# Kernel tuning notes

Measured on AMD Instinct MI355X. Metric: run time of the kernel, lower is better.

## Reference

```python
import jax, jax.numpy as jnp
import numpy as np
import math

SCALE = 64.0
MARGIN = 0.5
EPS = 1e-07
COS_M = math.cos(MARGIN)
SIN_M = math.sin(MARGIN)
THRESHOLD = math.cos(math.pi - MARGIN)
MM = math.sin(math.pi - MARGIN) * MARGIN

N, D, C = 512, 512, 100000


def setup_inputs() -> dict:
    key = jax.random.key(0)
    k1, k2, k3 = jax.random.split(key, 3)
    x = jax.random.normal(k1, (N, D), dtype=jnp.float32)
    weight = jax.random.normal(k2, (C, D), dtype=jnp.float32)
    t = jnp.zeros((1,), dtype=jnp.float32)
    target = jax.random.randint(k3, (N,), 0, C, dtype=jnp.int64)
    return {"x": x, "weight": weight, "t": t, "target": target}


def reference(x, weight, t, target):
    # normalized linear -> cosine similarities [N, C]
    xn = x / jnp.linalg.norm(x, axis=1, keepdims=True)
    wn = weight / jnp.linalg.norm(weight, axis=1, keepdims=True)
    cos_theta = jnp.clip(jnp.einsum('nd,cd->nc', xn, wn), -1.0 + EPS, 1.0 - EPS)

    rows = jnp.arange(cos_theta.shape[0])
    target_logit = cos_theta[rows, target][:, None]            # [N, 1]
    sin_theta = jnp.sqrt(1.0 - target_logit * target_logit)
    cos_theta_m = target_logit * COS_M - sin_theta * SIN_M      # cos(theta + m)

    mask = cos_theta > cos_theta_m                              # hard examples
    final_target_logit = jnp.where(target_logit > THRESHOLD,
                                   cos_theta_m,
                                   target_logit - MM)

    # EMA buffer update (no-grad in torch)
    t_new = jax.lax.stop_gradient(target_logit.mean() * 0.01 + 0.99 * t)  # [1]

    # hard-example re-weighting: cos * (t + cos) where mask
    cos_theta = jnp.where(mask, cos_theta * (t_new[0] + cos_theta), cos_theta)
    # scatter margin-adjusted target logit into target column
    cos_theta = cos_theta.at[rows, target].set(final_target_logit[:, 0])

    logits = cos_theta * SCALE
    # cross entropy (mean)
    logp = jax.nn.log_softmax(logits, axis=-1)
    loss = -jnp.mean(logp[rows, target])
    return loss
```

## Files before the change

### kernel.cpp

```cpp
#include <hip/hip_runtime.h>
#include <hip/hip_bf16.h>
#include <stdint.h>

#define N_ROWS 512
#define D_DIM  512
#define C_CLS  100000

#define SCALE_F    64.0f
#define EPS_F      1e-7f
#define COS_M_F    0.8775825618903728f
#define SIN_M_F    0.4794255386042030f
#define THRESH_F  -0.8775825618903728f
#define MM_F       0.2397127693021015f
#define FIXMAX_F   65.0f

#define NC  64
#define NG2 1564

#define XN8_OFF    0
#define TL_OFF     (XN8_OFF + 512*512)
#define CTM_OFF    (TL_OFF + 2048)
#define FTL_OFF    (CTM_OFF + 2048)
#define TNEW_OFF   (FTL_OFF + 2048)
#define XNORM_OFF  (TNEW_OFF + 256)
#define PSUM_OFF   (XNORM_OFF + 2048)
#define LOSSI_OFF  (PSUM_OFF + NG2*512*4)

typedef __attribute__((ext_vector_type(4))) float f32x4;

#define GLOAD_LDS16(gp, lp) \
    __builtin_amdgcn_global_load_lds((const __attribute__((address_space(1))) void*)(gp), \
                                     (__attribute__((address_space(3))) void*)(lp), 16, 0, 0)

#if defined(__has_builtin)
#if __has_builtin(__builtin_amdgcn_cvt_pk_fp8_f32)
#define HAVE_CVT_FP8 1
#endif
#endif

__device__ inline unsigned char f2e4m3(float f) {
    union { float f; unsigned u; } a; a.f = f;
    unsigned s = (a.u >> 24) & 0x80u;
    float af = fabsf(f);
    if (af < 0.015625f) {
        int q = (int)(af * 512.0f + 0.5f);
        return (unsigned char)(s | (unsigned)q);
    }
    unsigned x = a.u & 0x7FFFFFFFu;
    unsigned r = x + 0x000FFFFFu + ((x >> 20) & 1u);
    int ec = (int)(r >> 23) - 127 + 7;
    unsigned m = (r >> 20) & 7u;
    if (ec > 15 || (ec == 15 && m == 7u)) return (unsigned char)(s | 0x7Eu);
    return (unsigned char)(s | ((unsigned)ec << 3) | m);
}

__device__ inline unsigned pack4_fp8(float f0, float f1, float f2, float f3) {
#ifdef HAVE_CVT_FP8
    int q = __builtin_amdgcn_cvt_pk_fp8_f32(f0, f1, 0, false);
    q     = __builtin_amdgcn_cvt_pk_fp8_f32(f2, f3, q, true);
    return (unsigned)q;
#else
    union { unsigned char b[4]; unsigned u; } u;
    u.b[0]=f2e4m3(f0); u.b[1]=f2e4m3(f1); u.b[2]=f2e4m3(f2); u.b[3]=f2e4m3(f3);
    return u.u;
#endif
}

__device__ inline uint2 pack8_fp8(float f0, float f1, float f2, float f3,
                                  float f4, float f5, float f6, float f7) {
    uint2 r;
    r.x = pack4_fp8(f0, f1, f2, f3);
    r.y = pack4_fp8(f4, f5, f6, f7);
    return r;
}

__device__ inline float wave_sum64(float v) {
    #pragma unroll
    for (int m = 1; m < 64; m <<= 1) v += __shfl_xor(v, m);
    return v;
}

__global__ void k_xnorm_fp8(const float* __restrict__ x,
                            unsigned char* __restrict__ xn8,
                            float* __restrict__ xnorm) {
    int row = blockIdx.x;
    int lane = threadIdx.x;
    const float* xr = x + row * D_DIM + lane * 8;
    float4 v0 = *(const float4*)(xr);
    float4 v1 = *(const float4*)(xr + 4);
    float s = v0.x*v0.x + v0.y*v0.y + v0.z*v0.z + v0.w*v0.w
            + v1.x*v1.x + v1.y*v1.y + v1.z*v1.z + v1.w*v1.w;
    s = wave_sum64(s);
    float nrm = sqrtf(s);
    if (lane == 0) xnorm[row] = nrm;
    float inv = 1.0f / nrm;
    uint2 q = pack8_fp8(v0.x*inv, v0.y*inv, v0.z*inv, v0.w*inv,
                        v1.x*inv, v1.y*inv, v1.z*inv, v1.w*inv);
    *(uint2*)(xn8 + row * D_DIM + lane * 8) = q;
}

__global__ void k_tlogit(const float* __restrict__ x, const float* __restrict__ w,
                         const float* __restrict__ xnorm,
                         const int* __restrict__ target,
                         float* __restrict__ tl, float* __restrict__ ctm,
                         float* __restrict__ ftl) {
    int row = blockIdx.x;
    int lane = threadIdx.x;
    int tgt = target[row];
    const float* xr = x + row * D_DIM + lane * 8;
    const float* wr = w + (size_t)tgt * D_DIM + lane * 8;
    float4 a0 = *(const float4*)(xr),     a1 = *(const float4*)(xr + 4);
    float4 b0 = *(const float4*)(wr),     b1 = *(const float4*)(wr + 4);
    float s = a0.x*b0.x + a0.y*b0.y + a0.z*b0.z + a0.w*b0.w
            + a1.x*b1.x + a1.y*b1.y + a1.z*b1.z + a1.w*b1.w;
    float q = b0.x*b0.x + b0.y*b0.y + b0.z*b0.z + b0.w*b0.w
            + b1.x*b1.x + b1.y*b1.y + b1.z*b1.z + b1.w*b1.w;
    s = wave_sum64(s);
    q = wave_sum64(q);
    if (lane == 0) {
        float c = s / (xnorm[row] * sqrtf(q));
        c = fminf(fmaxf(c, -1.0f + EPS_F), 1.0f - EPS_F);
        float sn = sqrtf(fmaxf(1.0f - c * c, 0.0f));
        float cm = c * COS_M_F - sn * SIN_M_F;
        tl[row]  = c;
        ctm[row] = cm;
        ftl[row] = (c > THRESH_F) ? cm : (c - MM_F);
    }
}

__global__ void k_tnew(const float* __restrict__ tl, const float* __restrict__ t,
                       float* __restrict__ tnew) {
    __shared__ float s[512];
    int tid = threadIdx.x;
    s[tid] = tl[tid];
    __syncthreads();
    for (int off = 256; off > 0; off >>= 1) {
        if (tid < off) s[tid] += s[tid + off];
        __syncthreads();
    }
    if (tid == 0) tnew[0] = (s[0] / 512.0f) * 0.01f + 0.99f * t[0];
}

__global__ __launch_bounds__(512, 4) void k_fused(
        const unsigned char* __restrict__ xn8,
        const float* __restrict__ w,
        const int* __restrict__ target,
        const float* __restrict__ ctm,
        const float* __restrict__ ftl,
        const float* __restrict__ tnew,
        float* __restrict__ psum) {
    __shared__ unsigned char As[2][512 * 64];
    __shared__ unsigned char Bs[2][64 * 64];
    __shared__ float invS[64];
    __shared__ int   tgt_s[512];
    __shared__ float ctm_s[512];
    __shared__ float ftl_s[512];

    int bx = blockIdx.x;
    int cb = bx * NC;
    int tid = threadIdx.x;
    int lane = tid & 63, wid = tid >> 6;
    int fr = lane & 15, rgrp = lane >> 4;
    int wrow = wid * 64;

    tgt_s[tid] = target[tid];
    ctm_s[tid] = ctm[tid];
    ftl_s[tid] = ftl[tid];
    float tn = tnew[0];

    int brow  = tid >> 3;
    int bslot = tid & 7;
    int bclass = cb + brow;
    bool brvalid = (bclass < C_CLS);
    const float* bsrc = w + (size_t)(brvalid ? bclass : 0) * D_DIM + bslot * 8;

    float sumsq = 0.0f;
    int bwaddr = brow * 64 + ((bslot * 8) ^ ((brow & 3) << 4));

    #define STAGE_A(kk, buf)                                                  \
        do {                                                                  \
            _Pragma("unroll")                                                 \
            for (int c = 0; c < 4; ++c) {                                     \
                int lo = c * 8192 + wid * 1024;             \
                int o  = lo + lane * 16;                                      \
                int row = o >> 6, b = o & 63;                                 \
                GLOAD_LDS16(xn8 + (size_t)row * 512 + (kk) * 64               \
                                + (b ^ ((row & 3) << 4)),                     \
                            (char*)As[buf] + lo);                             \
            }                                                                 \
        } while (0)

    #define WRITE_B(va, vb, buf)                                              \
        do {                                                                  \
            sumsq += va.x*va.x + va.y*va.y + va.z*va.z + va.w*va.w            \
                   + vb.x*vb.x + vb.y*vb.y + vb.z*vb.z + vb.w*vb.w;           \
            uint2 pk_;                                                        \
            pk_.x = pack4_fp8(va.x, va.y, va.z, va.w);                        \
            pk_.y = pack4_fp8(vb.x, vb.y, vb.z, vb.w);                        \
            *(uint2*)(&Bs[buf][bwaddr]) = pk_;                                \
        } while (0)

    __builtin_amdgcn_sched_barrier(0);
    float4 v0a = *(const float4*)(bsrc);
    float4 v0b = *(const float4*)(bsrc + 4);
    STAGE_A(0, 0);
    __builtin_amdgcn_sched_barrier(0);
    float4 rv_next0 = *(const float4*)(bsrc + 1 * 64);
    float4 rv_next1 = *(const float4*)(bsrc + 1 * 64 + 4);
    float4 rv_far0  = *(const float4*)(bsrc + 2 * 64);
    float4 rv_far1  = *(const float4*)(bsrc + 2 * 64 + 4);
    WRITE_B(v0a, v0b, 0);
    asm volatile("s_waitcnt vmcnt(4) lgkmcnt(0)" ::: "memory");
    __builtin_amdgcn_sched_barrier(0);
    __builtin_amdgcn_s_barrier();
    __builtin_amdgcn_sched_barrier(0);

    f32x4 acc[4][4];
    #pragma unroll
    for (int m = 0; m < 4; m++)
        #pragma unroll
        for (int j = 0; j < 4; j++)
            acc[m][j] = (f32x4){0.f, 0.f, 0.f, 0.f};

    union LL { uint2 u; long long ll; };
    int akey = (fr & 3) << 4;

    #pragma unroll
    for (int kk = 0; kk < 8; ++kk) {
        int cur = kk & 1;
        if (kk < 7) {
            STAGE_A(kk + 1, cur ^ 1);
            __builtin_amdgcn_sched_barrier(0);
            WRITE_B(rv_next0, rv_next1, cur ^ 1);
            rv_next0 = rv_far0;
            rv_next1 = rv_far1;
            if (kk < 5) {
                rv_far0 = *(const float4*)(bsrc + (kk + 3) * 64);
                rv_far1 = *(const float4*)(bsrc + (kk + 3) * 64 + 4);
            }
        }
        #pragma unroll
        for (int sub = 0; sub < 2; ++sub) {
            uint2 af[4], bf[4];
            int soff = (sub * 32 + rgrp * 8) ^ akey;
            #pragma unroll
            for (int m = 0; m < 4; m++)
                af[m] = *(const uint2*)(&As[cur][(wrow + m * 16 + fr) * 64 + soff]);
            #pragma unroll
            for (int j = 0; j < 4; j++)
                bf[j] = *(const uint2*)(&Bs[cur][(j * 16 + fr) * 64 + soff]);
            __builtin_amdgcn_s_setprio(1);
            #pragma unroll
            for (int m = 0; m < 4; m++)
                #pragma unroll
                for (int j = 0; j < 4; j++) {
                    LL a, b;
                    a.u = af[m];
                    b.u = bf[j];
                    acc[m][j] = __builtin_amdgcn_mfma_f32_16x16x32_fp8_fp8(
                                    a.ll, b.ll, acc[m][j], 0, 0, 0);
                }
            __builtin_amdgcn_s_setprio(0);
        }
        if (kk < 7) {
            if (kk < 5)
                asm volatile("s_waitcnt vmcnt(2) lgkmcnt(0)" ::: "memory");
            else
                asm volatile("s_waitcnt vmcnt(0) lgkmcnt(0)" ::: "memory");
            __builtin_amdgcn_sched_barrier(0);
            __builtin_amdgcn_s_barrier();
            __builtin_amdgcn_sched_barrier(0);
        }
    }
    #undef STAGE_A
    #undef WRITE_B

    float s2 = sumsq;
    s2 += __shfl_xor(s2, 1);
    s2 += __shfl_xor(s2, 2);
    s2 += __shfl_xor(s2, 4);
    if (bslot == 0) invS[brow] = rsqrtf(s2);
    __syncthreads();

    float inv[4];
    bool cvalid[4];
    #pragma unroll
    for (int j = 0; j < 4; j++) {
        inv[j] = invS[j * 16 + fr];
        cvalid[j] = (cb + j * 16 + fr) < C_CLS;
    }
    #pragma unroll
    for (int m = 0; m < 4; m++) {
        #pragma unroll
        for (int reg = 0; reg < 4; reg++) {
            int rl = wrow + m * 16 + rgrp * 4 + reg;
            int tr = tgt_s[rl];
            float cm = ctm_s[rl];
            float ft = ftl_s[rl];
            float sm = 0.0f;
            #pragma unroll
            for (int j = 0; j < 4; j++) {
                int col = cb + j * 16 + fr;
                float c = acc[m][j][reg] * inv[j];
                c = fminf(fmaxf(c, -1.0f + EPS_F), 1.0f - EPS_F);
                float v = (c > cm) ? c * (tn + c) : c;
                v *= SCALE_F;
                v = (col == tr) ? ft * SCALE_F : v;
                v = cvalid[j] ? v : -3.0e38f;
                sm += __expf(v - FIXMAX_F);
            }
            #pragma unroll
            for (int msk = 1; msk < 16; msk <<= 1) sm += __shfl_xor(sm, msk);
            if (fr == 0) psum[(size_t)bx * 512 + rl] = sm;
        }
    }
}

__global__ void k_rowlse_fix(const float* __restrict__ psum,
                             const float* __restrict__ ftl,
                             float* __restrict__ lossi) {
    int row = blockIdx.x, tid = threadIdx.x;
    float S = 0.0f;
    for (int nb = tid; nb < NG2; nb += 256) S += psum[(size_t)nb * 512 + row];
    __shared__ float sS[256];
    sS[tid] = S;
    __syncthreads();
    for (int off = 128; off > 0; off >>= 1) {
        if (tid < off) sS[tid] += sS[tid + off];
        __syncthreads();
    }
    if (tid == 0) lossi[row] = logf(sS[0]) + FIXMAX_F - SCALE_F * ftl[row];
}

__global__ void k_final(const float* __restrict__ lossi, float* __restrict__ out) {
    __shared__ float s[512];
    int tid = threadIdx.x;
    s[tid] = lossi[tid];
    __syncthreads();
    for (int off = 256; off > 0; off >>= 1) {
        if (tid < off) s[tid] += s[tid + off];
        __syncthreads();
    }
    if (tid == 0) out[0] = s[0] / 512.0f;
}

extern "C" void kernel_launch(void* const* d_in, const int* in_sizes, int n_in,
                              void* d_out, int out_size, void* d_ws, size_t ws_size,
                              hipStream_t stream) {
    const float* x      = (const float*)d_in[0];
    const float* w      = (const float*)d_in[1];
    const float* t      = (const float*)d_in[2];
    const int*   target = (const int*)d_in[3];

    char* ws = (char*)d_ws;
    unsigned char* xn8  = (unsigned char*)(ws + XN8_OFF);
    float* tl    = (float*)(ws + TL_OFF);
    float* ctm   = (float*)(ws + CTM_OFF);
    float* ftl   = (float*)(ws + FTL_OFF);
    float* tnew  = (float*)(ws + TNEW_OFF);
    float* xnorm = (float*)(ws + XNORM_OFF);
    float* psum  = (float*)(ws + PSUM_OFF);
    float* lossi = (float*)(ws + LOSSI_OFF);
    float* out   = (float*)d_out;

    k_xnorm_fp8<<<dim3(N_ROWS), dim3(64), 0, stream>>>(x, xn8, xnorm);
    k_tlogit<<<dim3(N_ROWS), dim3(64), 0, stream>>>(x, w, xnorm, target, tl, ctm, ftl);
    k_tnew<<<dim3(1), dim3(512), 0, stream>>>(tl, t, tnew);
    k_fused<<<dim3(NG2), dim3(512), 0, stream>>>(xn8, w, target, ctm, ftl, tnew, psum);
    k_rowlse_fix<<<dim3(N_ROWS), dim3(256), 0, stream>>>(psum, ftl, lossi);
    k_final<<<dim3(1), dim3(512), 0, stream>>>(lossi, out);
}
```

Measured before the change: 122.8 us.

## Merge prep kernels, fold EMA reduction into GEMM, pad B tile

Merges the x-normalisation and target-logit kernels into one prep kernel and drops the separate t_new reduction kernel. Each GEMM block now recomputes the mean of the target logits with wave reductions, which removes two launches and their serialisation gaps. The per-row target/ctm/ftl values are read from global memory in the epilogue instead of being staged in shared memory. The B tile switches from an XOR swizzle to a 72-byte padded row stride. The trade-off is redundant per-block reduction work and uncached-looking global loads in the epilogue.

```diff
diff --git a/kernel.cpp b/kernel.cpp
--- a/kernel.cpp
+++ b/kernel.cpp
@@ -21,9 +21,7 @@
 #define TL_OFF     (XN8_OFF + 512*512)
 #define CTM_OFF    (TL_OFF + 2048)
 #define FTL_OFF    (CTM_OFF + 2048)
-#define TNEW_OFF   (FTL_OFF + 2048)
-#define XNORM_OFF  (TNEW_OFF + 256)
-#define PSUM_OFF   (XNORM_OFF + 2048)
+#define PSUM_OFF   (FTL_OFF + 2048)
 #define LOSSI_OFF  (PSUM_OFF + NG2*512*4)
 
 typedef __attribute__((ext_vector_type(4))) float f32x4;
@@ -66,59 +64,43 @@
 #endif
 }
 
-__device__ inline uint2 pack8_fp8(float f0, float f1, float f2, float f3,
-                                  float f4, float f5, float f6, float f7) {
-    uint2 r;
-    r.x = pack4_fp8(f0, f1, f2, f3);
-    r.y = pack4_fp8(f4, f5, f6, f7);
-    return r;
-}
-
 __device__ inline float wave_sum64(float v) {
     #pragma unroll
     for (int m = 1; m < 64; m <<= 1) v += __shfl_xor(v, m);
     return v;
 }
 
-__global__ void k_xnorm_fp8(const float* __restrict__ x,
-                            unsigned char* __restrict__ xn8,
-                            float* __restrict__ xnorm) {
+__global__ void k_prep(const float* __restrict__ x, const float* __restrict__ w,
+                       const int* __restrict__ target,
+                       unsigned char* __restrict__ xn8,
+                       float* __restrict__ tl, float* __restrict__ ctm,
+                       float* __restrict__ ftl) {
     int row = blockIdx.x;
     int lane = threadIdx.x;
     const float* xr = x + row * D_DIM + lane * 8;
     float4 v0 = *(const float4*)(xr);
     float4 v1 = *(const float4*)(xr + 4);
-    float s = v0.x*v0.x + v0.y*v0.y + v0.z*v0.z + v0.w*v0.w
-            + v1.x*v1.x + v1.y*v1.y + v1.z*v1.z + v1.w*v1.w;
-    s = wave_sum64(s);
-    float nrm = sqrtf(s);
-    if (lane == 0) xnorm[row] = nrm;
+    float sx = v0.x*v0.x + v0.y*v0.y + v0.z*v0.z + v0.w*v0.w
+             + v1.x*v1.x + v1.y*v1.y + v1.z*v1.z + v1.w*v1.w;
+    sx = wave_sum64(sx);
+    float nrm = sqrtf(sx);
     float inv = 1.0f / nrm;
-    uint2 q = pack8_fp8(v0.x*inv, v0.y*inv, v0.z*inv, v0.w*inv,
-                        v1.x*inv, v1.y*inv, v1.z*inv, v1.w*inv);
-    *(uint2*)(xn8 + row * D_DIM + lane * 8) = q;
-}
-
-__global__ void k_tlogit(const float* __restrict__ x, const float* __restrict__ w,
-                         const float* __restrict__ xnorm,
-                         const int* __restrict__ target,
-                         float* __restrict__ tl, float* __restrict__ ctm,
-                         float* __restrict__ ftl) {
-    int row = blockIdx.x;
-    int lane = threadIdx.x;
+    uint2 q8;
+    q8.x = pack4_fp8(v0.x*inv, v0.y*inv, v0.z*inv, v0.w*inv);
+    q8.y = pack4_fp8(v1.x*inv, v1.y*inv, v1.z*inv, v1.w*inv);
+    *(uint2*)(xn8 + row * D_DIM + lane * 8) = q8;
+
     int tgt = target[row];
-    const float* xr = x + row * D_DIM + lane * 8;
     const float* wr = w + (size_t)tgt * D_DIM + lane * 8;
-    float4 a0 = *(const float4*)(xr),     a1 = *(const float4*)(xr + 4);
-    float4 b0 = *(const float4*)(wr),     b1 = *(const float4*)(wr + 4);
-    float s = a0.x*b0.x + a0.y*b0.y + a0.z*b0.z + a0.w*b0.w
-            + a1.x*b1.x + a1.y*b1.y + a1.z*b1.z + a1.w*b1.w;
+    float4 b0 = *(const float4*)(wr), b1 = *(const float4*)(wr + 4);
+    float s = v0.x*b0.x + v0.y*b0.y + v0.z*b0.z + v0.w*b0.w
+            + v1.x*b1.x + v1.y*b1.y + v1.z*b1.z + v1.w*b1.w;
     float q = b0.x*b0.x + b0.y*b0.y + b0.z*b0.z + b0.w*b0.w
             + b1.x*b1.x + b1.y*b1.y + b1.z*b1.z + b1.w*b1.w;
     s = wave_sum64(s);
     q = wave_sum64(q);
     if (lane == 0) {
-        float c = s / (xnorm[row] * sqrtf(q));
+        float c = s / (nrm * sqrtf(q));
         c = fminf(fmaxf(c, -1.0f + EPS_F), 1.0f - EPS_F);
         float sn = sqrtf(fmaxf(1.0f - c * c, 0.0f));
         float cm = c * COS_M_F - sn * SIN_M_F;
@@ -128,33 +110,18 @@
     }
 }
 
-__global__ void k_tnew(const float* __restrict__ tl, const float* __restrict__ t,
-                       float* __restrict__ tnew) {
-    __shared__ float s[512];
-    int tid = threadIdx.x;
-    s[tid] = tl[tid];
-    __syncthreads();
-    for (int off = 256; off > 0; off >>= 1) {
-        if (tid < off) s[tid] += s[tid + off];
-        __syncthreads();
-    }
-    if (tid == 0) tnew[0] = (s[0] / 512.0f) * 0.01f + 0.99f * t[0];
-}
-
 __global__ __launch_bounds__(512, 4) void k_fused(
         const unsigned char* __restrict__ xn8,
         const float* __restrict__ w,
         const int* __restrict__ target,
         const float* __restrict__ ctm,
         const float* __restrict__ ftl,
-        const float* __restrict__ tnew,
+        const float* __restrict__ tl,
+        const float* __restrict__ t,
         float* __restrict__ psum) {
     __shared__ unsigned char As[2][512 * 64];
-    __shared__ unsigned char Bs[2][64 * 64];
+    __shared__ unsigned char Bs[2][64 * 72];
     __shared__ float invS[64];
-    __shared__ int   tgt_s[512];
-    __shared__ float ctm_s[512];
-    __shared__ float ftl_s[512];
 
     int bx = blockIdx.x;
     int cb = bx * NC;
@@ -163,10 +130,19 @@
     int fr = lane & 15, rgrp = lane >> 4;
     int wrow = wid * 64;
 
-    tgt_s[tid] = target[tid];
-    ctm_s[tid] = ctm[tid];
-    ftl_s[tid] = ftl[tid];
-    float tn = tnew[0];
+    {
+        float v = tl[tid];
+        v = wave_sum64(v);
+        if (lane == 0) invS[wid] = v;
+    }
+    __syncthreads();
+    float tn;
+    {
+        float s8 = invS[0] + invS[1] + invS[2] + invS[3]
+                 + invS[4] + invS[5] + invS[6] + invS[7];
+        tn = (s8 / 512.0f) * 0.01f + 0.99f * t[0];
+    }
+    __syncthreads();
 
     int brow  = tid >> 3;
     int bslot = tid & 7;
@@ -175,7 +151,7 @@
     const float* bsrc = w + (size_t)(brvalid ? bclass : 0) * D_DIM + bslot * 8;
 
     float sumsq = 0.0f;
-    int bwaddr = brow * 64 + ((bslot * 8) ^ ((brow & 3) << 4));
+    int bwaddr = brow * 72 + bslot * 8;
 
     #define STAGE_A(kk, buf)                                                  \
         do {                                                                  \
@@ -243,12 +219,13 @@
         for (int sub = 0; sub < 2; ++sub) {
             uint2 af[4], bf[4];
             int soff = (sub * 32 + rgrp * 8) ^ akey;
+            int bcol = sub * 32 + rgrp * 8;
             #pragma unroll
             for (int m = 0; m < 4; m++)
                 af[m] = *(const uint2*)(&As[cur][(wrow + m * 16 + fr) * 64 + soff]);
             #pragma unroll
             for (int j = 0; j < 4; j++)
-                bf[j] = *(const uint2*)(&Bs[cur][(j * 16 + fr) * 64 + soff]);
+                bf[j] = *(const uint2*)(&Bs[cur][(j * 16 + fr) * 72 + bcol]);
             __builtin_amdgcn_s_setprio(1);
             #pragma unroll
             for (int m = 0; m < 4; m++)
@@ -294,9 +271,9 @@
         #pragma unroll
         for (int reg = 0; reg < 4; reg++) {
             int rl = wrow + m * 16 + rgrp * 4 + reg;
-            int tr = tgt_s[rl];
-            float cm = ctm_s[rl];
-            float ft = ftl_s[rl];
+            int tr = target[rl];
+            float cm = ctm[rl];
+            float ft = ftl[rl];
             float sm = 0.0f;
             #pragma unroll
             for (int j = 0; j < 4; j++) {
@@ -357,16 +334,12 @@
     float* tl    = (float*)(ws + TL_OFF);
     float* ctm   = (float*)(ws + CTM_OFF);
     float* ftl   = (float*)(ws + FTL_OFF);
-    float* tnew  = (float*)(ws + TNEW_OFF);
-    float* xnorm = (float*)(ws + XNORM_OFF);
     float* psum  = (float*)(ws + PSUM_OFF);
     float* lossi = (float*)(ws + LOSSI_OFF);
     float* out   = (float*)d_out;
 
-    k_xnorm_fp8<<<dim3(N_ROWS), dim3(64), 0, stream>>>(x, xn8, xnorm);
-    k_tlogit<<<dim3(N_ROWS), dim3(64), 0, stream>>>(x, w, xnorm, target, tl, ctm, ftl);
-    k_tnew<<<dim3(1), dim3(512), 0, stream>>>(tl, t, tnew);
-    k_fused<<<dim3(NG2), dim3(512), 0, stream>>>(xn8, w, target, ctm, ftl, tnew, psum);
+    k_prep<<<dim3(N_ROWS), dim3(64), 0, stream>>>(x, w, target, xn8, tl, ctm, ftl);
+    k_fused<<<dim3(NG2), dim3(512), 0, stream>>>(xn8, w, target, ctm, ftl, tl, t, psum);
     k_rowlse_fix<<<dim3(N_ROWS), dim3(256), 0, stream>>>(psum, ftl, lossi);
     k_final<<<dim3(1), dim3(512), 0, stream>>>(lossi, out);
 }
```

After: 135.7 us. 10.5% more time.
